# Performance work log

Measured on AMD Instinct MI355X. Metric: run time of the kernel, lower is better.

Reference implementation:

```python
import jax, jax.numpy as jnp
import numpy as np

WINDOW_SIZE = 7
L = 255.0
C1 = (0.01 * L) ** 2
C2 = (0.03 * L) ** 2


def _box_filter(x, window):
    # x: [B,1,H,W], window: [1,1,k,k] (uniform 1/k^2). VALID conv, groups=1.
    return jax.lax.conv_general_dilated(
        x, window, window_strides=(1, 1), padding='VALID',
        dimension_numbers=('NCHW', 'OIHW', 'NCHW'))


def setup_inputs() -> dict:
    key = jax.random.key(0)
    k1, k2 = jax.random.split(key)
    shape = (16, 1, 1080, 1920)
    img1 = jax.random.uniform(k1, shape, dtype=jnp.float32) * L
    img2 = jax.random.uniform(k2, shape, dtype=jnp.float32) * L
    window = jnp.ones((1, 1, WINDOW_SIZE, WINDOW_SIZE), dtype=jnp.float32) / (WINDOW_SIZE * WINDOW_SIZE)
    return {"img1": img1, "img2": img2, "window": window}


def reference(img1, img2, window):
    mu1 = _box_filter(img1, window)
    mu2 = _box_filter(img2, window)
    mu1_sq = mu1 * mu1
    mu2_sq = mu2 * mu2
    mu1_mu2 = mu1 * mu2
    sigma1_sq = _box_filter(img1 * img1, window) - mu1_sq
    sigma2_sq = _box_filter(img2 * img2, window) - mu2_sq
    sigma12 = _box_filter(img1 * img2, window) - mu1_mu2
    v1 = 2.0 * sigma12 + C2
    v2 = sigma1_sq + sigma2_sq + C2
    ssim_map = (2.0 * mu1_mu2 + C1) * v1 / ((mu1_sq + mu2_sq + C1) * v2)
    return jnp.mean(ssim_map)
```

## Files before the change

kernel.cpp:

```cpp
#include <hip/hip_runtime.h>


constexpr int W_IN = 1920, H_IN = 1080;
constexpr int WOUT = W_IN - 6;
constexpr int HOUT = H_IN - 6;
constexpr int NBATCH = 16;
constexpr int RCOLS = 26;
constexpr int TW = 16 * RCOLS;
constexpr int TH = 43;
constexpr int NBX = 5, NBY = 25;
constexpr int NBLK = NBX * NBY * NBATCH;

constexpr float C1f = 6.5025f;
constexpr float C2f = 58.5225f;
constexpr float INV49 = 1.0f / 49.0f;

template <int CTRL>
__device__ __forceinline__ float dpp_shl(float v) {
  return __int_as_float(__builtin_amdgcn_update_dpp(
      0, __float_as_int(v), CTRL, 0xf, 0xf, true));
}
#define SHL1(v) dpp_shl<0x101>(v)
#define SHL2(v) dpp_shl<0x102>(v)
#define SHL3(v) dpp_shl<0x103>(v)

__global__ __attribute__((amdgpu_flat_work_group_size(256, 256)))
void ssim_kernel(const float* __restrict__ img1, const float* __restrict__ img2,
                 double* __restrict__ partial) {
  __shared__ float wsum[4];

  const int t = threadIdx.x;
  const int lane = t & 63;
  const int sub = lane & 15;
  const int xr = blockIdx.x * TW + (t >> 4) * RCOLS;
  const int y0 = blockIdx.y * TH;
  const size_t ib = (size_t)blockIdx.z * (size_t)(H_IN * W_IN);
  const float* __restrict__ p1 = img1 + ib;
  const float* __restrict__ p2 = img2 + ib;

  const int c0 = xr + 2 * sub;
  const int gcol = min(c0, W_IN - 2);
  const bool pv = sub < 13;
  const bool m0 = pv && (c0 + 0 < WOUT);
  const bool m1 = pv && (c0 + 1 < WOUT);

  float V1_0 = 0.f, V1_1 = 0.f;
  float V2_0 = 0.f, V2_1 = 0.f;
  float V3_0 = 0.f, V3_1 = 0.f;
  float V4_0 = 0.f, V4_1 = 0.f;
  float V5_0 = 0.f, V5_1 = 0.f;
  float accv = 0.f;

  float2 Aa = *(const float2*)(p1 + (size_t)y0 * W_IN + gcol);
  float2 Ab = *(const float2*)(p2 + (size_t)y0 * W_IN + gcol);
  float2 Ba, Bb, Pa, Pb, Qa, Qb;
  int gyn = y0 + 1;
  int gyo = y0 + 1;
  int oy = y0;

#define EPI1(VA, VB, VAA, VBB, VAB, MASK)                                   \
  {                                                                         \
    const float mu1 = (VA) * INV49, mu2 = (VB) * INV49;                     \
    const float mu1s = mu1 * mu1, mu2s = mu2 * mu2, mu12 = mu1 * mu2;       \
    const float sg1 = fmaf((VAA), INV49, -mu1s);                            \
    const float sg2 = fmaf((VBB), INV49, -mu2s);                            \
    const float sg12 = fmaf((VAB), INV49, -mu12);                           \
    const float v1 = fmaf(2.f, sg12, C2f);                                  \
    const float v2 = sg1 + sg2 + C2f;                                       \
    const float num = fmaf(2.f, mu12, C1f) * v1;                            \
    const float den = (mu1s + mu2s + C1f) * v2;                             \
    const float ss = num * __builtin_amdgcn_rcpf(den);                      \
    accv += (MASK) ? ss : 0.f;                                              \
  }

#define HQ(Q)                                                               \
    const float s1_##Q = SHL1(H##Q);                                        \
    const float s2_##Q = SHL2(H##Q);                                        \
    const float s3_##Q = SHL3(H##Q);                                        \
    const float f3_##Q = SHL3(V##Q##_0);                                    \
    const float sh_##Q = s1_##Q + s2_##Q;                                   \
    const float h0_##Q = (H##Q + sh_##Q) + f3_##Q;                          \
    const float h1_##Q = (V##Q##_1 + sh_##Q) + s3_##Q;

#define VUPD_ADD(CAa, CAb)                                                  \
    V1_0 += CAa.x;                   V1_1 += CAa.y;                         \
    V2_0 += CAb.x;                   V2_1 += CAb.y;                         \
    V3_0 = fmaf(CAa.x, CAa.x, V3_0); V3_1 = fmaf(CAa.y, CAa.y, V3_1);       \
    V4_0 = fmaf(CAb.x, CAb.x, V4_0); V4_1 = fmaf(CAb.y, CAb.y, V4_1);       \
    V5_0 = fmaf(CAa.x, CAb.x, V5_0); V5_1 = fmaf(CAa.y, CAb.y, V5_1);

#define VUPD_SUB(COa, COb)                                                  \
    V1_0 -= COa.x;                     V1_1 -= COa.y;                       \
    V2_0 -= COb.x;                     V2_1 -= COb.y;                       \
    V3_0 = fmaf(-COa.x, COa.x, V3_0);  V3_1 = fmaf(-COa.y, COa.y, V3_1);    \
    V4_0 = fmaf(-COb.x, COb.x, V4_0);  V4_1 = fmaf(-COb.y, COb.y, V4_1);    \
    V5_0 = fmaf(-COa.x, COb.x, V5_0);  V5_1 = fmaf(-COa.y, COb.y, V5_1);

#define DO_EPI_BLOCK                                                        \
    if (oy < HOUT) {                                                        \
      const float H1 = V1_0 + V1_1;                                         \
      const float H2 = V2_0 + V2_1;                                         \
      const float H3 = V3_0 + V3_1;                                         \
      const float H4 = V4_0 + V4_1;                                         \
      const float H5 = V5_0 + V5_1;                                         \
      HQ(1) HQ(2) HQ(3) HQ(4) HQ(5)                                         \
      EPI1(h0_1, h0_2, h0_3, h0_4, h0_5, m0)                                \
      EPI1(h1_1, h1_2, h1_3, h1_4, h1_5, m1)                                \
    }                                                                       \
    ++oy;

#define STEPW(CAa, CAb, NAa, NAb, DO_EPI)                                   \
  {                                                                         \
    NAa = *(const float2*)(p1 + (size_t)gyn * W_IN + gcol);                 \
    NAb = *(const float2*)(p2 + (size_t)gyn * W_IN + gcol);                 \
    gyn = min(gyn + 1, H_IN - 1);                                           \
    VUPD_ADD(CAa, CAb)                                                      \
    if (DO_EPI) { DO_EPI_BLOCK }                                            \
  }

#define STEPM(CAa, CAb, NAa, NAb, COa, COb, NOa, NOb)                       \
  {                                                                         \
    NAa = *(const float2*)(p1 + (size_t)gyn * W_IN + gcol);                 \
    NAb = *(const float2*)(p2 + (size_t)gyn * W_IN + gcol);                 \
    gyn = min(gyn + 1, H_IN - 1);                                           \
    {                                                                       \
      const int yo = min(gyo, H_IN - 1);                                    \
      NOa = *(const float2*)(p1 + (size_t)yo * W_IN + gcol);                \
      NOb = *(const float2*)(p2 + (size_t)yo * W_IN + gcol);                \
      ++gyo;                                                                \
    }                                                                       \
    VUPD_ADD(CAa, CAb)                                                      \
    VUPD_SUB(COa, COb)                                                      \
    DO_EPI_BLOCK                                                            \
  }

  STEPW(Aa, Ab, Ba, Bb, false)
  STEPW(Ba, Bb, Aa, Ab, false)
  STEPW(Aa, Ab, Ba, Bb, false)
  STEPW(Ba, Bb, Aa, Ab, false)
  STEPW(Aa, Ab, Ba, Bb, false)
  STEPW(Ba, Bb, Aa, Ab, false)
  STEPW(Aa, Ab, Ba, Bb, true)
  Pa = *(const float2*)(p1 + (size_t)y0 * W_IN + gcol);
  Pb = *(const float2*)(p2 + (size_t)y0 * W_IN + gcol);
  for (int gp = 0; gp < 21; ++gp) {
    STEPM(Ba, Bb, Aa, Ab, Pa, Pb, Qa, Qb)
    STEPM(Aa, Ab, Ba, Bb, Qa, Qb, Pa, Pb)
  }
#undef STEPM
#undef STEPW
#undef DO_EPI_BLOCK
#undef VUPD_SUB
#undef VUPD_ADD
#undef HQ
#undef EPI1

#pragma unroll
  for (int off = 32; off > 0; off >>= 1) accv += __shfl_down(accv, off);
  if ((t & 63) == 0) wsum[t >> 6] = accv;
  __syncthreads();
  if (t == 0) {
    const int bid = blockIdx.x + NBX * (blockIdx.y + NBY * blockIdx.z);
    partial[bid] = (double)wsum[0] + (double)wsum[1] +
                   (double)wsum[2] + (double)wsum[3];
  }
}

__global__ __launch_bounds__(256)
void finalize_kernel(const double* __restrict__ partial,
                     float* __restrict__ out) {
  const int tid = threadIdx.x;
  double s = 0.0;
  for (int i = tid; i < NBLK; i += 256) s += partial[i];
#pragma unroll
  for (int off = 32; off > 0; off >>= 1) s += __shfl_down(s, off);
  __shared__ double ws[4];
  if ((tid & 63) == 0) ws[tid >> 6] = s;
  __syncthreads();
  if (tid == 0) {
    const double tot = ws[0] + ws[1] + ws[2] + ws[3];
    out[0] = (float)(tot / ((double)NBATCH * (double)HOUT * (double)WOUT));
  }
}

extern "C" void kernel_launch(void* const* d_in, const int* in_sizes, int n_in,
                              void* d_out, int out_size, void* d_ws, size_t ws_size,
                              hipStream_t stream) {
  const float* img1 = (const float*)d_in[0];
  const float* img2 = (const float*)d_in[1];
  double* partial = (double*)d_ws;
  dim3 grid(NBX, NBY, NBATCH);
  hipLaunchKernelGGL(ssim_kernel, grid, dim3(256), 0, stream, img1, img2,
                     partial);
  hipLaunchKernelGGL(finalize_kernel, dim3(1), dim3(256), 0, stream, partial,
                     (float*)d_out);
}
```

Measured before the change: 295.7 us.

## Deepen row-load prefetch to four stages with sched barriers and retile height

Replaces the one-row-ahead double-buffered loads with a four-deep ring of incoming and outgoing row registers, so global loads are issued several iterations before use. Sched barriers pin each step's loads ahead of the arithmetic. The tile height drops from 43 to 41 rows with 27 blocks in y so the loop divides evenly into groups of four. This hides more memory latency at the cost of extra VGPRs and slightly more halo rows reloaded across tiles.

```diff
diff --git a/kernel.cpp b/kernel.cpp
--- a/kernel.cpp
+++ b/kernel.cpp
@@ -7,8 +7,8 @@
 constexpr int NBATCH = 16;
 constexpr int RCOLS = 26;
 constexpr int TW = 16 * RCOLS;
-constexpr int TH = 43;
-constexpr int NBX = 5, NBY = 25;
+constexpr int TH = 41;
+constexpr int NBX = 5, NBY = 27;
 constexpr int NBLK = NBX * NBY * NBATCH;
 
 constexpr float C1f = 6.5025f;
@@ -51,12 +51,19 @@
   float V5_0 = 0.f, V5_1 = 0.f;
   float accv = 0.f;
 
-  float2 Aa = *(const float2*)(p1 + (size_t)y0 * W_IN + gcol);
-  float2 Ab = *(const float2*)(p2 + (size_t)y0 * W_IN + gcol);
-  float2 Ba, Bb, Pa, Pb, Qa, Qb;
-  int gyn = y0 + 1;
-  int gyo = y0 + 1;
+  float2 N0a, N0b, N1a, N1b, N2a, N2b, N3a, N3b;
+  float2 O0a, O0b, O1a, O1b, O2a, O2b, O3a, O3b;
+
+  int gyn = y0 + 10;
+  int gyo = y0 + 3;
   int oy = y0;
+
+#define LOAD2(da, db, yexpr)                                                \
+  {                                                                         \
+    const int yy_ = min((yexpr), H_IN - 1);                                 \
+    da = *(const float2*)(p1 + (size_t)yy_ * W_IN + gcol);                  \
+    db = *(const float2*)(p2 + (size_t)yy_ * W_IN + gcol);                  \
+  }
 
 #define EPI1(VA, VB, VAA, VBB, VAB, MASK)                                   \
   {                                                                         \
@@ -109,51 +116,56 @@
     }                                                                       \
     ++oy;
 
-#define STEPW(CAa, CAb, NAa, NAb, DO_EPI)                                   \
-  {                                                                         \
-    NAa = *(const float2*)(p1 + (size_t)gyn * W_IN + gcol);                 \
-    NAb = *(const float2*)(p2 + (size_t)gyn * W_IN + gcol);                 \
-    gyn = min(gyn + 1, H_IN - 1);                                           \
-    VUPD_ADD(CAa, CAb)                                                      \
-    if (DO_EPI) { DO_EPI_BLOCK }                                            \
-  }
-
-#define STEPM(CAa, CAb, NAa, NAb, COa, COb, NOa, NOb)                       \
-  {                                                                         \
-    NAa = *(const float2*)(p1 + (size_t)gyn * W_IN + gcol);                 \
-    NAb = *(const float2*)(p2 + (size_t)gyn * W_IN + gcol);                 \
-    gyn = min(gyn + 1, H_IN - 1);                                           \
-    {                                                                       \
-      const int yo = min(gyo, H_IN - 1);                                    \
-      NOa = *(const float2*)(p1 + (size_t)yo * W_IN + gcol);                \
-      NOb = *(const float2*)(p2 + (size_t)yo * W_IN + gcol);                \
-      ++gyo;                                                                \
-    }                                                                       \
-    VUPD_ADD(CAa, CAb)                                                      \
-    VUPD_SUB(COa, COb)                                                      \
+#define WSTEP(C, L, yrow)                                                   \
+  {                                                                         \
+    LOAD2(L##a, L##b, yrow)                                                 \
+    __builtin_amdgcn_sched_barrier(0);                                      \
+    VUPD_ADD(C##a, C##b)                                                    \
+  }
+#define WSTEPO(C, L, O, yrow, yold)                                         \
+  {                                                                         \
+    LOAD2(L##a, L##b, yrow)                                                 \
+    LOAD2(O##a, O##b, yold)                                                 \
+    __builtin_amdgcn_sched_barrier(0);                                      \
+    VUPD_ADD(C##a, C##b)                                                    \
+  }
+#define MSTEP(C, LN, OS, OL)                                                \
+  {                                                                         \
+    LOAD2(LN##a, LN##b, gyn) ++gyn;                                         \
+    LOAD2(OL##a, OL##b, gyo) ++gyo;                                         \
+    __builtin_amdgcn_sched_barrier(0);                                      \
+    VUPD_ADD(C##a, C##b)                                                    \
+    VUPD_SUB(OS##a, OS##b)                                                  \
     DO_EPI_BLOCK                                                            \
   }
 
-  STEPW(Aa, Ab, Ba, Bb, false)
-  STEPW(Ba, Bb, Aa, Ab, false)
-  STEPW(Aa, Ab, Ba, Bb, false)
-  STEPW(Ba, Bb, Aa, Ab, false)
-  STEPW(Aa, Ab, Ba, Bb, false)
-  STEPW(Ba, Bb, Aa, Ab, false)
-  STEPW(Aa, Ab, Ba, Bb, true)
-  Pa = *(const float2*)(p1 + (size_t)y0 * W_IN + gcol);
-  Pb = *(const float2*)(p2 + (size_t)y0 * W_IN + gcol);
-  for (int gp = 0; gp < 21; ++gp) {
-    STEPM(Ba, Bb, Aa, Ab, Pa, Pb, Qa, Qb)
-    STEPM(Aa, Ab, Ba, Bb, Qa, Qb, Pa, Pb)
-  }
-#undef STEPM
-#undef STEPW
+  LOAD2(N0a, N0b, y0 + 0)
+  LOAD2(N1a, N1b, y0 + 1)
+  LOAD2(N2a, N2b, y0 + 2)
+  __builtin_amdgcn_sched_barrier(0);
+  WSTEP(N0, N3, y0 + 3)
+  WSTEP(N1, N0, y0 + 4)
+  WSTEP(N2, N1, y0 + 5)
+  WSTEP(N3, N2, y0 + 6)
+  WSTEPO(N0, N3, O0, y0 + 7, y0 + 0)
+  WSTEPO(N1, N0, O1, y0 + 8, y0 + 1)
+  WSTEPO(N2, N1, O2, y0 + 9, y0 + 2)
+  DO_EPI_BLOCK
+  for (int g = 0; g < 10; ++g) {
+    MSTEP(N3, N2, O0, O3)
+    MSTEP(N0, N3, O1, O0)
+    MSTEP(N1, N0, O2, O1)
+    MSTEP(N2, N1, O3, O2)
+  }
+#undef MSTEP
+#undef WSTEPO
+#undef WSTEP
 #undef DO_EPI_BLOCK
 #undef VUPD_SUB
 #undef VUPD_ADD
 #undef HQ
 #undef EPI1
+#undef LOAD2
 
 #pragma unroll
   for (int off = 32; off > 0; off >>= 1) accv += __shfl_down(accv, off);
```

Measured after the change: 300.8 us. About the same (+1.7%).
